# Kernel optimization log

Measured on AMD Instinct MI355X. Metric: run time of the kernel, lower is better.

Reference implementation:

```python
import jax, jax.numpy as jnp
import numpy as np

N = 100000   # nodes
E = 1600000  # edges (avg in-degree 16)
D = 64       # feature dim (dim_in = dim_out)


def setup_inputs() -> dict:
    key = jax.random.key(0)
    k1, k2, k3, k4, k5, k6 = jax.random.split(key, 6)
    h = jax.random.normal(k1, (N, D), dtype=jnp.float32)
    src = jax.random.randint(k2, (E,), 0, N, dtype=jnp.int32)
    dst = jax.random.randint(k3, (E,), 0, N, dtype=jnp.int32)
    scale = 1.0 / np.sqrt(D).astype(np.float32)
    W1 = jax.random.normal(k4, (D, D), dtype=jnp.float32) * scale  # Linear(dim_in, dim_out, bias=False)
    W2 = jax.random.normal(k5, (D, D), dtype=jnp.float32) * scale  # Linear(dim_out, dim_out, bias=True)
    b2 = jax.random.normal(k6, (D,), dtype=jnp.float32) * scale
    return {"h": h, "src": src, "dst": dst, "W1": W1, "W2": W2, "b2": b2}


def reference(h, src, dst, W1, W2, b2):
    # GINConv with 'max' aggregation, eps = 0 (DGL default, not learned):
    #   out = MLP( h + max_{(u->v) in E} h[u] )
    msgs = h[src]  # [E, D] gather of source features
    agg = jax.ops.segment_max(msgs, dst, num_segments=N)  # [N, D]
    # Nodes with no in-edges: DGL's max-reduce yields zeros, segment_max yields -inf.
    deg = jax.ops.segment_sum(jnp.ones((E,), dtype=h.dtype), dst, num_segments=N)  # [N]
    agg = jnp.where(deg[:, None] > 0, agg, jnp.zeros((), dtype=h.dtype))
    x = h + agg                       # (1 + eps) * h_dst + agg, eps = 0
    y = jnp.maximum(x @ W1.T, 0.0)    # Linear(no bias) + ReLU
    return y @ W2.T + b2              # Linear(bias)
```

## Files before the change

kernel.cpp:

```cpp
#include <hip/hip_runtime.h>
#include <math.h>

#define NN 100000
#define EE 1600000
#define D 64

#define BSH 7
#define BSIZE 128
#define NBUK ((NN + BSIZE - 1) / BSIZE)
#define CAP 2296
#define EPB 8192
#define AST 65


__device__ __forceinline__ unsigned short encbf(float x) {
    unsigned int b = __float_as_uint(x);
    unsigned short u = (unsigned short)((b + 0x7FFFu + ((b >> 16) & 1u)) >> 16);
    return u ^ ((u & 0x8000u) ? 0xFFFFu : 0x8000u);
}

__global__ void kPrep(const float* __restrict__ h, unsigned short* __restrict__ hb,
                      const float* __restrict__ W1, float* __restrict__ W1T,
                      const float* __restrict__ W2, float* __restrict__ W2T,
                      int* __restrict__ gcur) {
    int i = blockIdx.x * blockDim.x + threadIdx.x;
    const float4* h4 = (const float4*)h;
    ushort4* hb4 = (ushort4*)hb;
    for (int idx = i; idx < NN * D / 4; idx += gridDim.x * blockDim.x) {
        float4 v = h4[idx];
        ushort4 r;
        r.x = encbf(v.x); r.y = encbf(v.y); r.z = encbf(v.z); r.w = encbf(v.w);
        hb4[idx] = r;
    }
    if (i < D * D) {
        int k = i >> 6, j = i & 63;
        W1T[i] = W1[j * D + k];
        W2T[i] = W2[j * D + k];
    }
    int z = i - D * D;
    if (z >= 0 && z < NBUK) gcur[z] = 0;
}

__global__ void __launch_bounds__(256) kA_scatter(const int* __restrict__ src,
                                                  const int* __restrict__ dst,
                                                  int* __restrict__ gcur,
                                                  int* __restrict__ bdata) {
    __shared__ int lcnt[NBUK];
    __shared__ int lcur[NBUK];
    const int t = threadIdx.x;
    for (int i = t; i < NBUK; i += 256) lcnt[i] = 0;
    __syncthreads();
    const int e0 = blockIdx.x * EPB;
    int dc[32];
#pragma unroll
    for (int k = 0; k < 32; k++) {
        int e = e0 + k * 256 + t;
        int d = -1;
        if (e < EE) {
            d = dst[e];
            atomicAdd(&lcnt[d >> BSH], 1);
        }
        dc[k] = d;
    }
    __syncthreads();
    for (int i = t; i < NBUK; i += 256)
        if (lcnt[i]) lcur[i] = atomicAdd(&gcur[i], lcnt[i]);
    __syncthreads();
#pragma unroll
    for (int k = 0; k < 32; k++) {
        int e = e0 + k * 256 + t;
        if (e < EE) {
            int d = dc[k];
            int bk = d >> BSH;
            int pos = atomicAdd(&lcur[bk], 1);
            if (pos < CAP) bdata[bk * CAP + pos] = (src[e] << BSH) | (d & (BSIZE - 1));
        }
    }
}

__global__ void __launch_bounds__(512) kC_fused(const float* __restrict__ h,
                                                const unsigned short* __restrict__ hb,
                                                const int* __restrict__ gcur,
                                                const int* __restrict__ bdata,
                                                const float* __restrict__ W1T,
                                                const float* __restrict__ W2T,
                                                const float* __restrict__ b2,
                                                float* __restrict__ out) {
    __shared__ unsigned int acc[BSIZE * AST];
    float* fac = (float*)acc;
    const int t = threadIdx.x;
    const int b = blockIdx.x;
    for (int i = t; i < BSIZE * AST; i += 512) acc[i] = 0u;
    __syncthreads();

    int cnt = gcur[b];
    if (cnt > CAP) cnt = CAP;
    const int wave = t >> 6, lane = t & 63;
    const int base = b * CAP;
    const int oct = lane >> 3;
    const int fb = (lane & 7) * 8;
    const char* hbB = (const char*)hb;
    for (int i0 = wave * 64; i0 < cnt; i0 += 8 * 64) {
        int rem = cnt - i0;
        if (rem > 64) rem = 64;
        int entry = 0;
        if (lane < rem) entry = bdata[base + i0 + lane];
        if (rem == 64) {
            uint4 u[8];
            int ro[8];
#pragma unroll
            for (int g = 0; g < 8; g++) {
                int e = __shfl(entry, g * 8 + oct, 64);
                ro[g] = (e & (BSIZE - 1)) * AST + fb;
                u[g] = *(const uint4*)(hbB + (e & ~(BSIZE - 1)) + fb * 2);
            }
#pragma unroll
            for (int g = 0; g < 8; g++) {
                atomicMax(&acc[ro[g] + 0], u[g].x << 16);
                atomicMax(&acc[ro[g] + 1], u[g].x & 0xFFFF0000u);
                atomicMax(&acc[ro[g] + 2], u[g].y << 16);
                atomicMax(&acc[ro[g] + 3], u[g].y & 0xFFFF0000u);
                atomicMax(&acc[ro[g] + 4], u[g].z << 16);
                atomicMax(&acc[ro[g] + 5], u[g].z & 0xFFFF0000u);
                atomicMax(&acc[ro[g] + 6], u[g].w << 16);
                atomicMax(&acc[ro[g] + 7], u[g].w & 0xFFFF0000u);
            }
        } else {
            for (int j = 0; j < rem; j++) {
                int ej = __shfl(entry, j, 64);
                unsigned int k16 = *(const unsigned short*)(hbB + (ej & ~(BSIZE - 1)) + lane * 2);
                atomicMax(&acc[(ej & (BSIZE - 1)) * AST + lane], k16 << 16);
            }
        }
    }
    __syncthreads();

    for (int n = wave; n < BSIZE; n += 8) {
        int v = b * BSIZE + n;
        float x = 0.0f;
        if (v < NN) {
            unsigned int key = acc[n * AST + lane];
            float m = 0.0f;
            if (key != 0u) {
                unsigned int e16 = key >> 16;
                unsigned int b16 = (e16 & 0x8000u) ? (e16 ^ 0x8000u) : ((~e16) & 0xFFFFu);
                m = __uint_as_float(b16 << 16);
            }
            x = h[(size_t)v * D + lane] + m;
        }
        fac[n * AST + lane] = x;
    }
    __syncthreads();

    const int n = t & (BSIZE - 1);
    const int hq = __builtin_amdgcn_readfirstlane(t >> 7);
    const float* w1 = W1T + hq * 16;
    const float* w2 = W2T + hq * 16;
    float y[16];
#pragma unroll
    for (int jj = 0; jj < 16; jj++) y[jj] = 0.0f;
#pragma unroll 8
    for (int k = 0; k < D; k++) {
        float xk = fac[n * AST + k];
#pragma unroll
        for (int jj = 0; jj < 16; jj++)
            y[jj] = fmaf(xk, w1[k * D + jj], y[jj]);
    }
#pragma unroll
    for (int jj = 0; jj < 16; jj++) y[jj] = fmaxf(y[jj], 0.0f);
    __syncthreads();
#pragma unroll
    for (int jj = 0; jj < 16; jj++) fac[n * AST + hq * 16 + jj] = y[jj];
    __syncthreads();

    float o[16];
#pragma unroll
    for (int ii = 0; ii < 16; ii++) o[ii] = b2[hq * 16 + ii];
#pragma unroll 8
    for (int j = 0; j < D; j++) {
        float yj = fac[n * AST + j];
#pragma unroll
        for (int ii = 0; ii < 16; ii++)
            o[ii] = fmaf(yj, w2[j * D + ii], o[ii]);
    }
    int v = b * BSIZE + n;
    if (v < NN) {
        float4* op = (float4*)(out + (size_t)v * D + hq * 16);
#pragma unroll
        for (int c = 0; c < 4; c++)
            op[c] = make_float4(o[4 * c], o[4 * c + 1], o[4 * c + 2], o[4 * c + 3]);
    }
}

extern "C" void kernel_launch(void* const* d_in, const int* in_sizes, int n_in,
                              void* d_out, int out_size, void* d_ws, size_t ws_size,
                              hipStream_t stream) {
    const float* h   = (const float*)d_in[0];
    const int*   src = (const int*)d_in[1];
    const int*   dst = (const int*)d_in[2];
    const float* W1  = (const float*)d_in[3];
    const float* W2  = (const float*)d_in[4];
    const float* b2  = (const float*)d_in[5];
    float* out = (float*)d_out;

    int* ws = (int*)d_ws;
    int* gcur  = ws;
    int* bdata = ws + 784;
    float* W2T = (float*)(ws + 784 + NBUK * CAP);
    float* W1T = W2T + D * D;
    unsigned short* hb = (unsigned short*)(W1T + D * D);

    const int B = 256;
    kPrep<<<1024, B, 0, stream>>>(h, hb, W1, W1T, W2, W2T, gcur);
    kA_scatter<<<(EE + EPB - 1) / EPB, B, 0, stream>>>(src, dst, gcur, bdata);
    kC_fused<<<NBUK, 512, 0, stream>>>(h, hb, gcur, bdata, W1T, W2T, b2, out);
}
```

Baseline: 192.5 us.

## Sort bucket edges by destination and reduce max in registers with packed u16 max

Merges the prep and scatter kernels into one launch, with the counter zeroing moved to a memset. In the fused kernel each bucket's edges are counting-sorted by local destination in shared memory. Each 8-lane group then walks one node's source list and takes the max in registers using v_pk_max_u16 on packed bf16 keys. This removes the many shared-memory atomicMax operations per edge. In exchange it adds a shared-memory sort pass and load imbalance across lanes from the max-degree loop within each 64-lane wave.

Result: no change. 194.2 us (+0.9%).

```diff
diff --git a/kernel.cpp b/kernel.cpp
--- a/kernel.cpp
+++ b/kernel.cpp
@@ -10,6 +10,7 @@
 #define NBUK ((NN + BSIZE - 1) / BSIZE)
 #define CAP 2296
 #define EPB 8192
+#define SCATB ((EE + EPB - 1) / EPB)
 #define AST 65
 
 
@@ -19,136 +20,178 @@
     return u ^ ((u & 0x8000u) ? 0xFFFFu : 0x8000u);
 }
 
-__global__ void kPrep(const float* __restrict__ h, unsigned short* __restrict__ hb,
-                      const float* __restrict__ W1, float* __restrict__ W1T,
-                      const float* __restrict__ W2, float* __restrict__ W2T,
-                      int* __restrict__ gcur) {
-    int i = blockIdx.x * blockDim.x + threadIdx.x;
+__device__ __forceinline__ unsigned int pkmax(unsigned int a, unsigned int b) {
+    unsigned int d;
+    asm("v_pk_max_u16 %0, %1, %2" : "=v"(d) : "v"(a), "v"(b));
+    return d;
+}
+
+__global__ void __launch_bounds__(256) kAP(const float* __restrict__ h,
+                                           unsigned short* __restrict__ hb,
+                                           const float* __restrict__ W1, float* __restrict__ W1T,
+                                           const float* __restrict__ W2, float* __restrict__ W2T,
+                                           const int* __restrict__ src, const int* __restrict__ dst,
+                                           int* __restrict__ gcur, int* __restrict__ bdata) {
+    __shared__ int lcnt[NBUK];
+    __shared__ int lcur[NBUK];
+    const int t = threadIdx.x;
+    const int b = blockIdx.x;
+    if (b < SCATB) {
+        for (int i = t; i < NBUK; i += 256) lcnt[i] = 0;
+        __syncthreads();
+        const int e0 = b * EPB;
+        int dc[32];
+#pragma unroll
+        for (int k = 0; k < 32; k++) {
+            int e = e0 + k * 256 + t;
+            int d = -1;
+            if (e < EE) {
+                d = dst[e];
+                atomicAdd(&lcnt[d >> BSH], 1);
+            }
+            dc[k] = d;
+        }
+        __syncthreads();
+        for (int i = t; i < NBUK; i += 256)
+            if (lcnt[i]) lcur[i] = atomicAdd(&gcur[i], lcnt[i]);
+        __syncthreads();
+#pragma unroll
+        for (int k = 0; k < 32; k++) {
+            int e = e0 + k * 256 + t;
+            if (e < EE) {
+                int d2 = dc[k];
+                int bk = d2 >> BSH;
+                int pos = atomicAdd(&lcur[bk], 1);
+                if (pos < CAP) bdata[bk * CAP + pos] = (src[e] << BSH) | (d2 & (BSIZE - 1));
+            }
+        }
+    }
+    int gi = b * 256 + t;
     const float4* h4 = (const float4*)h;
     ushort4* hb4 = (ushort4*)hb;
-    for (int idx = i; idx < NN * D / 4; idx += gridDim.x * blockDim.x) {
+    for (int idx = gi; idx < NN * D / 4; idx += gridDim.x * 256) {
         float4 v = h4[idx];
         ushort4 r;
         r.x = encbf(v.x); r.y = encbf(v.y); r.z = encbf(v.z); r.w = encbf(v.w);
         hb4[idx] = r;
     }
-    if (i < D * D) {
-        int k = i >> 6, j = i & 63;
-        W1T[i] = W1[j * D + k];
-        W2T[i] = W2[j * D + k];
-    }
-    int z = i - D * D;
-    if (z >= 0 && z < NBUK) gcur[z] = 0;
-}
-
-__global__ void __launch_bounds__(256) kA_scatter(const int* __restrict__ src,
-                                                  const int* __restrict__ dst,
-                                                  int* __restrict__ gcur,
-                                                  int* __restrict__ bdata) {
-    __shared__ int lcnt[NBUK];
-    __shared__ int lcur[NBUK];
-    const int t = threadIdx.x;
-    for (int i = t; i < NBUK; i += 256) lcnt[i] = 0;
-    __syncthreads();
-    const int e0 = blockIdx.x * EPB;
-    int dc[32];
-#pragma unroll
-    for (int k = 0; k < 32; k++) {
-        int e = e0 + k * 256 + t;
-        int d = -1;
-        if (e < EE) {
-            d = dst[e];
-            atomicAdd(&lcnt[d >> BSH], 1);
-        }
-        dc[k] = d;
-    }
-    __syncthreads();
-    for (int i = t; i < NBUK; i += 256)
-        if (lcnt[i]) lcur[i] = atomicAdd(&gcur[i], lcnt[i]);
-    __syncthreads();
-#pragma unroll
-    for (int k = 0; k < 32; k++) {
-        int e = e0 + k * 256 + t;
-        if (e < EE) {
-            int d = dc[k];
-            int bk = d >> BSH;
-            int pos = atomicAdd(&lcur[bk], 1);
-            if (pos < CAP) bdata[bk * CAP + pos] = (src[e] << BSH) | (d & (BSIZE - 1));
-        }
-    }
-}
-
-__global__ void __launch_bounds__(512) kC_fused(const float* __restrict__ h,
-                                                const unsigned short* __restrict__ hb,
-                                                const int* __restrict__ gcur,
-                                                const int* __restrict__ bdata,
-                                                const float* __restrict__ W1T,
-                                                const float* __restrict__ W2T,
-                                                const float* __restrict__ b2,
-                                                float* __restrict__ out) {
+    if (gi < D * D) {
+        int k = gi >> 6, j = gi & 63;
+        W1T[gi] = W1[j * D + k];
+        W2T[gi] = W2[j * D + k];
+    }
+}
+
+__global__ void __launch_bounds__(512) kC2(const float* __restrict__ h,
+                                           const unsigned short* __restrict__ hb,
+                                           const int* __restrict__ gcur,
+                                           const int* __restrict__ bdata,
+                                           const float* __restrict__ W1T,
+                                           const float* __restrict__ W2T,
+                                           const float* __restrict__ b2,
+                                           float* __restrict__ out) {
     __shared__ unsigned int acc[BSIZE * AST];
+    __shared__ int deg[BSIZE];
+    __shared__ int scn[BSIZE];
+    __shared__ int cur[BSIZE];
     float* fac = (float*)acc;
+    unsigned int* elist = acc;
     const int t = threadIdx.x;
     const int b = blockIdx.x;
-    for (int i = t; i < BSIZE * AST; i += 512) acc[i] = 0u;
-    __syncthreads();
-
     int cnt = gcur[b];
     if (cnt > CAP) cnt = CAP;
+    const int base = b * CAP;
+
+    if (t < BSIZE) deg[t] = 0;
+    __syncthreads();
+    for (int i = t; i < cnt; i += 512)
+        atomicAdd(&deg[bdata[base + i] & (BSIZE - 1)], 1);
+    __syncthreads();
+    if (t < BSIZE) scn[t] = deg[t];
+    __syncthreads();
+    for (int s = 1; s < BSIZE; s <<= 1) {
+        int v = 0;
+        if (t < BSIZE) { v = scn[t]; if (t >= s) v += scn[t - s]; }
+        __syncthreads();
+        if (t < BSIZE) scn[t] = v;
+        __syncthreads();
+    }
+    if (t < BSIZE) cur[t] = scn[t] - deg[t];
+    __syncthreads();
+    for (int i = t; i < cnt; i += 512) {
+        int e = bdata[base + i];
+        int pos = atomicAdd(&cur[e & (BSIZE - 1)], 1);
+        elist[pos] = ((unsigned)e) >> BSH;
+    }
+    __syncthreads();
+
     const int wave = t >> 6, lane = t & 63;
-    const int base = b * CAP;
     const int oct = lane >> 3;
-    const int fb = (lane & 7) * 8;
+    const int fbyte = (lane & 7) * 16;
     const char* hbB = (const char*)hb;
-    for (int i0 = wave * 64; i0 < cnt; i0 += 8 * 64) {
-        int rem = cnt - i0;
-        if (rem > 64) rem = 64;
-        int entry = 0;
-        if (lane < rem) entry = bdata[base + i0 + lane];
-        if (rem == 64) {
-            uint4 u[8];
-            int ro[8];
-#pragma unroll
-            for (int g = 0; g < 8; g++) {
-                int e = __shfl(entry, g * 8 + oct, 64);
-                ro[g] = (e & (BSIZE - 1)) * AST + fb;
-                u[g] = *(const uint4*)(hbB + (e & ~(BSIZE - 1)) + fb * 2);
-            }
-#pragma unroll
-            for (int g = 0; g < 8; g++) {
-                atomicMax(&acc[ro[g] + 0], u[g].x << 16);
-                atomicMax(&acc[ro[g] + 1], u[g].x & 0xFFFF0000u);
-                atomicMax(&acc[ro[g] + 2], u[g].y << 16);
-                atomicMax(&acc[ro[g] + 3], u[g].y & 0xFFFF0000u);
-                atomicMax(&acc[ro[g] + 4], u[g].z << 16);
-                atomicMax(&acc[ro[g] + 5], u[g].z & 0xFFFF0000u);
-                atomicMax(&acc[ro[g] + 6], u[g].w << 16);
-                atomicMax(&acc[ro[g] + 7], u[g].w & 0xFFFF0000u);
-            }
+    unsigned int m[2][4];
+#pragma unroll
+    for (int p = 0; p < 2; ++p)
+#pragma unroll
+        for (int c = 0; c < 4; ++c) m[p][c] = 0u;
+
+#pragma unroll
+    for (int p = 0; p < 2; ++p) {
+        const int n8 = wave * 16 + p * 8 + oct;
+        const int dg = deg[n8];
+        const int of = scn[n8] - deg[n8];
+        int md = dg;
+        md = max(md, __shfl_xor(md, 8));
+        md = max(md, __shfl_xor(md, 16));
+        md = max(md, __shfl_xor(md, 32));
+#pragma unroll 4
+        for (int r = 0; r < md; ++r) {
+            if (r < dg) {
+                unsigned int sidx = elist[of + r];
+                const uint4 uu = *(const uint4*)(hbB + (size_t)sidx * 128 + fbyte);
+                m[p][0] = pkmax(m[p][0], uu.x);
+                m[p][1] = pkmax(m[p][1], uu.y);
+                m[p][2] = pkmax(m[p][2], uu.z);
+                m[p][3] = pkmax(m[p][3], uu.w);
+            }
+        }
+    }
+    __syncthreads();
+
+#pragma unroll
+    for (int p = 0; p < 2; ++p) {
+        const int n8 = wave * 16 + p * 8 + oct;
+        const int v = b * BSIZE + n8;
+        const int f0 = (lane & 7) * 8;
+        float x[8];
+#pragma unroll
+        for (int c = 0; c < 4; ++c) {
+            unsigned int w = m[p][c];
+            unsigned int klo = w & 0xFFFFu;
+            unsigned int khi = w >> 16;
+            float mlo = 0.0f, mhi = 0.0f;
+            if (klo) {
+                unsigned int bb = (klo & 0x8000u) ? (klo ^ 0x8000u) : ((~klo) & 0xFFFFu);
+                mlo = __uint_as_float(bb << 16);
+            }
+            if (khi) {
+                unsigned int bb = (khi & 0x8000u) ? (khi ^ 0x8000u) : ((~khi) & 0xFFFFu);
+                mhi = __uint_as_float(bb << 16);
+            }
+            x[2 * c] = mlo;
+            x[2 * c + 1] = mhi;
+        }
+        if (v < NN) {
+            const float4* hp = (const float4*)(h + (size_t)v * D + f0);
+            float4 a0 = hp[0], a1 = hp[1];
+            x[0] += a0.x; x[1] += a0.y; x[2] += a0.z; x[3] += a0.w;
+            x[4] += a1.x; x[5] += a1.y; x[6] += a1.z; x[7] += a1.w;
         } else {
-            for (int j = 0; j < rem; j++) {
-                int ej = __shfl(entry, j, 64);
-                unsigned int k16 = *(const unsigned short*)(hbB + (ej & ~(BSIZE - 1)) + lane * 2);
-                atomicMax(&acc[(ej & (BSIZE - 1)) * AST + lane], k16 << 16);
-            }
-        }
-    }
-    __syncthreads();
-
-    for (int n = wave; n < BSIZE; n += 8) {
-        int v = b * BSIZE + n;
-        float x = 0.0f;
-        if (v < NN) {
-            unsigned int key = acc[n * AST + lane];
-            float m = 0.0f;
-            if (key != 0u) {
-                unsigned int e16 = key >> 16;
-                unsigned int b16 = (e16 & 0x8000u) ? (e16 ^ 0x8000u) : ((~e16) & 0xFFFFu);
-                m = __uint_as_float(b16 << 16);
-            }
-            x = h[(size_t)v * D + lane] + m;
-        }
-        fac[n * AST + lane] = x;
+#pragma unroll
+            for (int j = 0; j < 8; ++j) x[j] = 0.0f;
+        }
+#pragma unroll
+        for (int j = 0; j < 8; ++j) fac[n8 * AST + f0 + j] = x[j];
     }
     __syncthreads();
 
@@ -210,8 +253,7 @@
     float* W1T = W2T + D * D;
     unsigned short* hb = (unsigned short*)(W1T + D * D);
 
-    const int B = 256;
-    kPrep<<<1024, B, 0, stream>>>(h, hb, W1, W1T, W2, W2T, gcur);
-    kA_scatter<<<(EE + EPB - 1) / EPB, B, 0, stream>>>(src, dst, gcur, bdata);
-    kC_fused<<<NBUK, 512, 0, stream>>>(h, hb, gcur, bdata, W1T, W2T, b2, out);
-}
+    hipMemsetAsync(gcur, 0, 784 * sizeof(int), stream);
+    kAP<<<1024, 256, 0, stream>>>(h, hb, W1, W1T, W2, W2T, src, dst, gcur, bdata);
+    kC2<<<NBUK, 512, 0, stream>>>(h, hb, gcur, bdata, W1T, W2T, b2, out);
+}
```
